# Kernel tuning notes

Hardware: AMD Instinct MI355X
Metric: run time of the kernel (lower is better)

## Reference

```python
import jax, jax.numpy as jnp
import numpy as np

EPS_BN = 1e-5
EPS_NORM = 1e-12
TEMPERATURE = 0.1
TEMPLATE_LAMBDA = 0.5
KERNEL_WIDTH = 5


def conv1d(x, w, b, pad):
    # x: (B, Cin, W), w: (Cout, Cin, K)
    y = jax.lax.conv_general_dilated(x, w, window_strides=(1,), padding=[(pad, pad)],
                                     dimension_numbers=('NCW', 'OIW', 'NCW'))
    return y + b[None, :, None]


def batchnorm(x, g, be):
    # training-mode BN: batch stats over (B, W), biased variance (as torch)
    m = jnp.mean(x, axis=(0, 2), keepdims=True)
    v = jnp.mean((x - m) ** 2, axis=(0, 2), keepdims=True)
    return g[None, :, None] * (x - m) * jax.lax.rsqrt(v + EPS_BN) + be[None, :, None]


def maxpool4(x):
    return jax.lax.reduce_window(x, -jnp.inf, jax.lax.max, (1, 1, 4), (1, 1, 4), 'VALID')


def adaptive_avg_pool1d(x, k):
    # faithful torch AdaptiveAvgPool1d bin boundaries
    W = x.shape[-1]
    outs = []
    for i in range(k):
        s = (i * W) // k
        e = -(-((i + 1) * W) // k)  # ceil
        outs.append(jnp.mean(x[..., s:e], axis=-1))
    return jnp.stack(outs, axis=-1)


def l2norm(x):
    n = jnp.linalg.norm(x, axis=-1, keepdims=True)
    return x / jnp.maximum(n, EPS_NORM)


def encoder(x, w1, b1, g1, be1, w2, b2, g2, be2, w3, b3, g3, be3):
    h = maxpool4(jax.nn.relu(batchnorm(conv1d(x, w1, b1, 8), g1, be1)))
    h = maxpool4(jax.nn.relu(batchnorm(conv1d(h, w2, b2, 8), g2, be2)))
    h = maxpool4(jax.nn.relu(batchnorm(conv1d(h, w3, b3, 8), g3, be3)))
    return h  # (B, C, W=L/64)


def template_head(h, tw1, tb1, tg1, tbe1, tw2, tb2, tg2, tbe2):
    k = jax.nn.relu(batchnorm(conv1d(h, tw1, tb1, 2), tg1, tbe1))
    k = jax.nn.relu(batchnorm(conv1d(k, tw2, tb2, 1), tg2, tbe2))
    return adaptive_avg_pool1d(k, KERNEL_WIDTH)  # (B, C, W_k)


def template_similarity(k, h):
    # Equivalent to the torch B*B*C grouped 'same' conv1d followed by
    # sum over channels and mean over positions: since the result is the
    # SUM over all output positions of a zero-padded cross-correlation,
    # it factorizes as einsum of k with shifted window-sums of h.
    k = k - jnp.mean(k, axis=-1, keepdims=True)
    k = l2norm(k)  # (B, C, Wk)
    h = h - jnp.mean(h, axis=-1, keepdims=True)
    h = l2norm(h)  # (B, C, W)
    Wk = k.shape[-1]
    W = h.shape[-1]
    pad = (Wk - 1) // 2  # padding='same' for odd kernel
    hp = jnp.pad(h, ((0, 0), (0, 0), (pad, pad)))
    # S[j,c,t] = sum_w hp[j,c,w+t]  for t in [0, Wk)
    S = jnp.stack([jnp.sum(hp[:, :, t:t + W], axis=-1) for t in range(Wk)], axis=-1)
    return jnp.einsum('ick,jck->ij', k, S) / W  # (B, B)


def infonce(sim):
    logp = jax.nn.log_softmax(sim / TEMPERATURE, axis=-1)
    return -jnp.mean(jnp.diagonal(logp))


def template_contrastive_loss(k1, k2):
    B = k1.shape[0]
    a = l2norm(k1.reshape(B, -1))
    b = l2norm(k2.reshape(B, -1))
    return infonce(jnp.matmul(a, b.T) * TEMPERATURE / TEMPERATURE) if False else infonce(jnp.matmul(a, b.T))


def setup_inputs() -> dict:
    key = jax.random.key(0)
    ks = jax.random.split(key, 12)
    B, L, C = 256, 8192, 64
    inp = {
        'x1': jax.random.normal(ks[0], (B, 1, L), dtype=jnp.float32),
        'x2': jax.random.normal(ks[1], (B, 1, L), dtype=jnp.float32),
        # encoder params
        'w1': jax.random.normal(ks[2], (16, 1, 17), dtype=jnp.float32) * 0.1,
        'b1': jnp.zeros((16,), jnp.float32),
        'g1': jnp.ones((16,), jnp.float32), 'be1': jnp.zeros((16,), jnp.float32),
        'w2': jax.random.normal(ks[3], (32, 16, 17), dtype=jnp.float32) * 0.05,
        'b2': jnp.zeros((32,), jnp.float32),
        'g2': jnp.ones((32,), jnp.float32), 'be2': jnp.zeros((32,), jnp.float32),
        'w3': jax.random.normal(ks[4], (C, 32, 17), dtype=jnp.float32) * 0.04,
        'b3': jnp.zeros((C,), jnp.float32),
        'g3': jnp.ones((C,), jnp.float32), 'be3': jnp.zeros((C,), jnp.float32),
        # template head params
        'tw1': jax.random.normal(ks[5], (C, C, 5), dtype=jnp.float32) * 0.05,
        'tb1': jnp.zeros((C,), jnp.float32),
        'tg1': jnp.ones((C,), jnp.float32), 'tbe1': jnp.zeros((C,), jnp.float32),
        'tw2': jax.random.normal(ks[6], (C, C, 3), dtype=jnp.float32) * 0.07,
        'tb2': jnp.zeros((C,), jnp.float32),
        'tg2': jnp.ones((C,), jnp.float32), 'tbe2': jnp.zeros((C,), jnp.float32),
    }
    return inp


def reference(x1, x2, w1, b1, g1, be1, w2, b2, g2, be2, w3, b3, g3, be3,
              tw1, tb1, tg1, tbe1, tw2, tb2, tg2, tbe2):
    enc = (w1, b1, g1, be1, w2, b2, g2, be2, w3, b3, g3, be3)
    th = (tw1, tb1, tg1, tbe1, tw2, tb2, tg2, tbe2)
    h1 = encoder(x1, *enc)
    h2 = encoder(x2, *enc)
    k1 = template_head(h1, *th)
    k2 = template_head(h2, *th)
    loss_matching = (infonce(template_similarity(k1, h2)) +
                     infonce(template_similarity(k2, h1))) / 2
    loss_template = template_contrastive_loss(k1, k2)
    return loss_matching + TEMPLATE_LAMBDA * loss_template
```

## Files before the change

### kernel.cpp

```cpp
#include <hip/hip_runtime.h>
#include <hip/hip_bf16.h>
#include <math.h>


#define BSZ2 512
#define NTHR 256

typedef __attribute__((ext_vector_type(8))) short bf16x8;
typedef __attribute__((ext_vector_type(4))) float f32x4;

static inline int ceil_divll(long long a, int b) { return (int)((a + b - 1) / b); }

__device__ __forceinline__ unsigned short f2bf(float f) {
    unsigned u = __float_as_uint(f);
    u = (u + 0x7FFFu + ((u >> 16) & 1u)) >> 16;
    return (unsigned short)u;
}
__device__ __forceinline__ float bflo(unsigned u) { return __uint_as_float(u << 16); }
__device__ __forceinline__ float bfhi(unsigned u) { return __uint_as_float(u & 0xFFFF0000u); }

template<int WT>
__global__ __launch_bounds__(256)
void conv1_mfma(const float* __restrict__ x1, const float* __restrict__ x2,
                const unsigned short* __restrict__ wpack1, const float* __restrict__ bias,
                unsigned short* __restrict__ outMax, unsigned short* __restrict__ outMin,
                float* __restrict__ partials)
{
    constexpr int W = 8192;
    constexpr int CHUNK = 4 * WT * 16;
    __shared__ float xs[CHUNK + 32];
    __shared__ float sred[4][16];
    __shared__ float ssred[4][16];

    const int tid = threadIdx.x;
    const int ntile = W / CHUNK;
    const int b = blockIdx.x / ntile;
    const int w0 = (blockIdx.x % ntile) * CHUNK;
    const float* xrow = (b < 256) ? x1 + (long long)b * W : x2 + (long long)(b - 256) * W;

    for (int i = tid; i < CHUNK + 32; i += 256) {
        const int gw = w0 - 8 + i;
        xs[i] = (gw >= 0 && gw < W) ? xrow[gw] : 0.f;
    }
    __syncthreads();

    const int lane = tid & 63, wave = tid >> 6;
    const int n = lane & 15, kq = lane >> 4;
    const bf16x8 a = *(const bf16x8*)(wpack1 + lane * 8);

    f32x4 acc[WT];
#pragma unroll
    for (int wt = 0; wt < WT; ++wt) { acc[wt][0]=0.f; acc[wt][1]=0.f; acc[wt][2]=0.f; acc[wt][3]=0.f; }

    const int base0 = wave * WT * 16 + n + kq * 8;
#pragma unroll
    for (int wt = 0; wt < WT; ++wt) {
        bf16x8 bv;
#pragma unroll
        for (int j = 0; j < 8; ++j) {
            __hip_bfloat16 h = __float2bfloat16(xs[base0 + wt * 16 + j]);
            bv[j] = *reinterpret_cast<const short*>(&h);
        }
        acc[wt] = __builtin_amdgcn_mfma_f32_16x16x32_bf16(bv, a, acc[wt], 0, 0, 0);
    }

    const float bi = bias[n];
    float s_ = 0.f, ss_ = 0.f;
#pragma unroll
    for (int wt = 0; wt < WT; ++wt) {
        float v[4];
#pragma unroll
        for (int e = 0; e < 4; ++e) {
            v[e] = acc[wt][e] + bi;
            s_ += v[e]; ss_ += v[e] * v[e];
        }
        const float mx = fmaxf(fmaxf(v[0], v[1]), fmaxf(v[2], v[3]));
        const float mn = fminf(fminf(v[0], v[1]), fminf(v[2], v[3]));
        const int wp = (w0 >> 2) + wave * WT * 4 + wt * 4 + kq;
        outMax[((long long)b * 2048 + wp) * 16 + n] = f2bf(mx);
        outMin[((long long)b * 2048 + wp) * 16 + n] = f2bf(mn);
    }
    s_  += __shfl_xor(s_, 16, 64);  s_  += __shfl_xor(s_, 32, 64);
    ss_ += __shfl_xor(ss_, 16, 64); ss_ += __shfl_xor(ss_, 32, 64);
    if (lane < 16) { sred[wave][n] = s_; ssred[wave][n] = ss_; }
    __syncthreads();
    if (tid < 16) {
        float sumv = 0.f, sumsq = 0.f;
#pragma unroll
        for (int wv = 0; wv < 4; ++wv) { sumv += sred[wv][tid]; sumsq += ssred[wv][tid]; }
        partials[((long long)blockIdx.x * 16 + tid) * 2 + 0] = sumv;
        partials[((long long)blockIdx.x * 16 + tid) * 2 + 1] = sumsq;
    }
}

template<int COUT>
__global__ void finalize2(const float* __restrict__ partials, int nblk_half, float invN,
                          const float* __restrict__ g, const float* __restrict__ be,
                          float* __restrict__ scale, float* __restrict__ shift)
{
    const int co = blockIdx.x;
    const int half = blockIdx.y;
    const float* P = partials + (size_t)half * nblk_half * COUT * 2;
    float s = 0.f, ss = 0.f;
    for (int i = threadIdx.x; i < nblk_half; i += NTHR) {
        s  += P[((long long)i * COUT + co) * 2 + 0];
        ss += P[((long long)i * COUT + co) * 2 + 1];
    }
    __shared__ float red[NTHR][2];
    red[threadIdx.x][0] = s; red[threadIdx.x][1] = ss;
    __syncthreads();
    for (int off = NTHR / 2; off > 0; off >>= 1) {
        if ((int)threadIdx.x < off) {
            red[threadIdx.x][0] += red[threadIdx.x + off][0];
            red[threadIdx.x][1] += red[threadIdx.x + off][1];
        }
        __syncthreads();
    }
    if (threadIdx.x == 0) {
        const float m = red[0][0] * invN;
        const float v = red[0][1] * invN - m * m;
        const float inv = rsqrtf(v + 1e-5f);
        const float sc = g[co] * inv;
        scale[half * COUT + co] = sc;
        shift[half * COUT + co] = be[co] - sc * m;
    }
}

template<int CIN, int KK, int DT, int NP, int S, int CT>
__device__ __forceinline__ void pack_one(int idx, const float* __restrict__ wgt,
                                         unsigned short* __restrict__ wp)
{
    const int j = idx & 7;
    const int l = (idx >> 3) & 63;
    int rest = idx >> 9;
    const int ct = rest % CT; rest /= CT;
    const int s = rest % S;
    const int p = rest / S;
    const int co = ct * 16 + (l & 15);
    const int k = (l >> 4) * 8 + j;
    int ci, t;
    if (DT == 2) { ci = k & (CIN - 1); t = p * 2 + (k >> 4); }
    else         { ci = s * 32 + k;    t = p; }
    float v = (t < KK) ? wgt[((long long)co * CIN + ci) * KK + t] : 0.f;
    wp[idx] = f2bf(v);
}

__global__ void build_all_wpacks(const float* __restrict__ w1, const float* __restrict__ w2,
                                 const float* __restrict__ w3,
                                 const float* __restrict__ tw1, const float* __restrict__ tw2,
                                 unsigned short* __restrict__ wp1,
                                 unsigned short* __restrict__ wp2, unsigned short* __restrict__ wp3,
                                 unsigned short* __restrict__ wpt1, unsigned short* __restrict__ wpt2)
{
    const int idx = blockIdx.x * NTHR + threadIdx.x;
    const int n1 = 512;
    const int n2 = 9 * 1 * 2 * 512;
    const int n3 = 17 * 1 * 4 * 512;
    const int nt1 = 5 * 2 * 4 * 512;
    const int nt2 = 3 * 2 * 4 * 512;
    if (idx < n1) {
        const int j = idx & 7, l = idx >> 3;
        const int co = l & 15, k = (l >> 4) * 8 + j;
        wp1[idx] = f2bf((k < 17) ? w1[co * 17 + k] : 0.f);
    }
    else if (idx < n1 + n2) pack_one<16, 17, 2, 9, 1, 2>(idx - n1, w2, wp2);
    else if (idx < n1 + n2 + n3) pack_one<32, 17, 1, 17, 1, 4>(idx - n1 - n2, w3, wp3);
    else if (idx < n1 + n2 + n3 + nt1) pack_one<64, 5, 1, 5, 2, 4>(idx - n1 - n2 - n3, tw1, wpt1);
    else if (idx < n1 + n2 + n3 + nt1 + nt2) pack_one<64, 3, 1, 3, 2, 4>(idx - n1 - n2 - n3 - nt1, tw2, wpt2);
}

template<int CIN, int COUT, int KK, int PAD, int DT, int NP, int S, int CT, int ST,
         int SRCM, int OUTM>
__global__ __launch_bounds__(256)
void conv_mfma2(const unsigned short* __restrict__ xA, const unsigned short* __restrict__ xB,
                const float* __restrict__ pscale, const float* __restrict__ pshift,
                const unsigned short* __restrict__ wpack, const float* __restrict__ bias,
                unsigned short* __restrict__ outA, unsigned short* __restrict__ outB,
                float* __restrict__ partials, int W)
{
    constexpr int CHUNK = 4 * ST * 16;
    constexpr int ROWB = CIN * 2 + 16;
    constexpr int ROWS = CHUNK + KK + (DT - 1) + 1;
    constexpr int DPR = CIN / 2;
    __shared__ __align__(16) unsigned char lx[ROWS * ROWB];
    __shared__ float sred[4][CT][16];
    __shared__ float ssred[4][CT][16];
    __shared__ float scb[(SRCM > 0) ? CIN : 1];
    __shared__ float shb[(SRCM > 0) ? CIN : 1];

    const int tid = threadIdx.x;
    const int ntile = W / CHUNK;
    const int b = blockIdx.x / ntile;
    const int tile = blockIdx.x % ntile;
    const int w0 = tile * CHUNK;

    if (SRCM > 0) {
        if (tid < CIN) {
            scb[tid] = pscale[(b >> 8) * CIN + tid];
            shb[tid] = pshift[(b >> 8) * CIN + tid];
        }
        __syncthreads();
    }

    for (int d = tid; d < ROWS * DPR; d += 256) {
        const int row = d / DPR;
        const int col = d % DPR;
        const int gw = w0 - PAD + row;
        unsigned v = 0;
        if (gw >= 0 && gw < W) {
            const long long src = ((long long)b * W + gw) * CIN + col * 2;
            if (SRCM == 0) {
                v = *(const unsigned*)(xA + src);
            } else {
                const unsigned va = *(const unsigned*)(xA + src);
                const float sc0 = scb[col * 2], sh0 = shb[col * 2];
                const float sc1 = scb[col * 2 + 1], sh1 = shb[col * 2 + 1];
                float f0, f1;
                if (SRCM == 1) {
                    const unsigned vb = *(const unsigned*)(xB + src);
                    f0 = fmaxf(fmaf(sc0, (sc0 > 0.f) ? bflo(va) : bflo(vb), sh0), 0.f);
                    f1 = fmaxf(fmaf(sc1, (sc1 > 0.f) ? bfhi(va) : bfhi(vb), sh1), 0.f);
                } else {
                    f0 = fmaxf(fmaf(sc0, bflo(va), sh0), 0.f);
                    f1 = fmaxf(fmaf(sc1, bfhi(va), sh1), 0.f);
                }
                v = (unsigned)f2bf(f0) | ((unsigned)f2bf(f1) << 16);
            }
        }
        *(unsigned*)(lx + row * ROWB + col * 4) = v;
    }
    __syncthreads();

    const int lane = tid & 63, wave = tid >> 6;
    const int n = lane & 15, kq = lane >> 4;
    int rowbase, cbyte;
    if (DT == 2) { rowbase = wave * ST * 16 + n + (kq >> 1); cbyte = (kq & 1) * 16; }
    else         { rowbase = wave * ST * 16 + n;             cbyte = kq * 16; }

    f32x4 acc[ST][CT];
#pragma unroll
    for (int st = 0; st < ST; ++st)
#pragma unroll
        for (int ct = 0; ct < CT; ++ct) { acc[st][ct][0]=0.f; acc[st][ct][1]=0.f; acc[st][ct][2]=0.f; acc[st][ct][3]=0.f; }

#pragma unroll
    for (int p = 0; p < NP; ++p) {
#pragma unroll
        for (int s = 0; s < S; ++s) {
            bf16x8 a[CT];
#pragma unroll
            for (int ct = 0; ct < CT; ++ct)
                a[ct] = *(const bf16x8*)(wpack + (((long long)(p * S + s) * CT + ct) * 64 + lane) * 8);
#pragma unroll
            for (int st = 0; st < ST; ++st) {
                const int r = rowbase + st * 16 + p * DT;
                const bf16x8 bf = *(const bf16x8*)(lx + r * ROWB + cbyte + s * 64);
#pragma unroll
                for (int ct = 0; ct < CT; ++ct)
                    acc[st][ct] = __builtin_amdgcn_mfma_f32_16x16x32_bf16(bf, a[ct], acc[st][ct], 0, 0, 0);
            }
        }
    }

    float s_[CT], ss_[CT];
#pragma unroll
    for (int ct = 0; ct < CT; ++ct) { s_[ct] = 0.f; ss_[ct] = 0.f; }

#pragma unroll
    for (int st = 0; st < ST; ++st) {
        const int wbase = w0 + wave * ST * 16 + st * 16 + kq * 4;
#pragma unroll
        for (int ct = 0; ct < CT; ++ct) {
            const float bi = bias[ct * 16 + n];
            float v[4];
#pragma unroll
            for (int e = 0; e < 4; ++e) {
                v[e] = acc[st][ct][e] + bi;
                s_[ct] += v[e];
                ss_[ct] += v[e] * v[e];
            }
            if (OUTM == 0) {
#pragma unroll
                for (int e = 0; e < 4; ++e)
                    outA[((long long)b * W + wbase + e) * COUT + ct * 16 + n] = f2bf(v[e]);
            } else {
                const float mx = fmaxf(fmaxf(v[0], v[1]), fmaxf(v[2], v[3]));
                const float mn = fminf(fminf(v[0], v[1]), fminf(v[2], v[3]));
                const long long o = ((long long)b * (W >> 2) + (wbase >> 2)) * COUT + ct * 16 + n;
                outA[o] = f2bf(mx);
                outB[o] = f2bf(mn);
            }
        }
    }
#pragma unroll
    for (int ct = 0; ct < CT; ++ct) {
        s_[ct]  += __shfl_xor(s_[ct], 16, 64);  s_[ct]  += __shfl_xor(s_[ct], 32, 64);
        ss_[ct] += __shfl_xor(ss_[ct], 16, 64); ss_[ct] += __shfl_xor(ss_[ct], 32, 64);
    }
    if (lane < 16) {
#pragma unroll
        for (int ct = 0; ct < CT; ++ct) { sred[wave][ct][n] = s_[ct]; ssred[wave][ct][n] = ss_[ct]; }
    }
    __syncthreads();
    if (tid < COUT) {
        const int ct = tid >> 4, nn = tid & 15;
        float sumv = 0.f, sumsq = 0.f;
#pragma unroll
        for (int wv = 0; wv < 4; ++wv) { sumv += sred[wv][ct][nn]; sumsq += ssred[wv][ct][nn]; }
        partials[((long long)blockIdx.x * COUT + tid) * 2 + 0] = sumv;
        partials[((long long)blockIdx.x * COUT + tid) * 2 + 1] = sumsq;
    }
}

__global__ void tail_pool_srow(const unsigned short* __restrict__ yT2b,
                               const float* __restrict__ scT2, const float* __restrict__ shT2,
                               const unsigned short* __restrict__ yMax3,
                               const unsigned short* __restrict__ yMin3,
                               const float* __restrict__ scS3, const float* __restrict__ shS3,
                               float* __restrict__ kn, float* __restrict__ ab,
                               float* __restrict__ Sv)
{
    __shared__ float hb[128][64];
    const int tid = threadIdx.x;
    if (blockIdx.x < BSZ2) {
        const int b = blockIdx.x;
        __shared__ float pk[320];
        __shared__ float red2[NTHR];
        const uint2* yd = (const uint2*)(yT2b + (long long)b * 128 * 64);
        for (int i = tid; i < 128 * 16; i += 256) {
            const int w = i >> 4, c4 = (i & 15) * 4;
            const float* scp = scT2 + (b >> 8) * 64 + c4;
            const float* shp = shT2 + (b >> 8) * 64 + c4;
            const uint2 v = yd[i];
            hb[w][c4 + 0] = fmaxf(fmaf(scp[0], bflo(v.x), shp[0]), 0.f);
            hb[w][c4 + 1] = fmaxf(fmaf(scp[1], bfhi(v.x), shp[1]), 0.f);
            hb[w][c4 + 2] = fmaxf(fmaf(scp[2], bflo(v.y), shp[2]), 0.f);
            hb[w][c4 + 3] = fmaxf(fmaf(scp[3], bfhi(v.y), shp[3]), 0.f);
        }
        __syncthreads();
        const int bs[5] = {0, 25, 51, 76, 102};
        const int be5[5] = {26, 52, 77, 103, 128};
        for (int o = tid; o < 320; o += 256) {
            const int cc = o & 63, bin = o >> 6;
            float acc = 0.f;
            for (int w = bs[bin]; w < be5[bin]; ++w) acc += hb[w][cc];
            pk[cc * 5 + bin] = acc / (float)(be5[bin] - bs[bin]);
        }
        __syncthreads();
        float n2p = pk[tid] * pk[tid];
        if (tid < 64) n2p += pk[256 + tid] * pk[256 + tid];
        red2[tid] = n2p;
        __syncthreads();
        for (int off = NTHR / 2; off > 0; off >>= 1) {
            if (tid < off) red2[tid] += red2[tid + off];
            __syncthreads();
        }
        const float nrm = fmaxf(sqrtf(red2[0]), 1e-12f);
        for (int i = tid; i < 320; i += 256) ab[(long long)b * 320 + i] = pk[i] / nrm;
        if (tid < 64) {
            const float* p = pk + tid * 5;
            float m = 0.f;
            for (int t = 0; t < 5; ++t) m += p[t];
            m *= 0.2f;
            float v[5]; float q = 0.f;
            for (int t = 0; t < 5; ++t) { v[t] = p[t] - m; q += v[t] * v[t]; }
            const float n = fmaxf(sqrtf(q), 1e-12f);
            float* o = kn + ((long long)b * 64 + tid) * 5;
            for (int t = 0; t < 5; ++t) o[t] = v[t] / n;
        }
    } else {
        __shared__ float red[4][64];
        __shared__ float mrow[64];
        const int b = blockIdx.x - BSZ2;
        const int c = tid & 63, grp = tid >> 6;
        const uint2* ya = (const uint2*)(yMax3 + (long long)b * 128 * 64);
        const uint2* yb = (const uint2*)(yMin3 + (long long)b * 128 * 64);
        for (int i = tid; i < 128 * 16; i += 256) {
            const int w = i >> 4, c4 = (i & 15) * 4;
            const float* scp = scS3 + (b >> 8) * 64 + c4;
            const float* shp = shS3 + (b >> 8) * 64 + c4;
            const uint2 va = ya[i], vb = yb[i];
            hb[w][c4 + 0] = fmaxf(fmaf(scp[0], (scp[0] > 0.f) ? bflo(va.x) : bflo(vb.x), shp[0]), 0.f);
            hb[w][c4 + 1] = fmaxf(fmaf(scp[1], (scp[1] > 0.f) ? bfhi(va.x) : bfhi(vb.x), shp[1]), 0.f);
            hb[w][c4 + 2] = fmaxf(fmaf(scp[2], (scp[2] > 0.f) ? bflo(va.y) : bflo(vb.y), shp[2]), 0.f);
            hb[w][c4 + 3] = fmaxf(fmaf(scp[3], (scp[3] > 0.f) ? bfhi(va.y) : bfhi(vb.y), shp[3]), 0.f);
        }
        __syncthreads();
        float s = 0.f;
        for (int w = grp * 32; w < grp * 32 + 32; ++w) s += hb[w][c];
        red[grp][c] = s;
        __syncthreads();
        if (tid < 64) mrow[tid] = (red[0][tid] + red[1][tid] + red[2][tid] + red[3][tid]) / 128.f;
        __syncthreads();
        const float m = mrow[c];
        float q = 0.f;
        for (int w = grp * 32; w < grp * 32 + 32; ++w) { const float d = hb[w][c] - m; q += d * d; }
        red[grp][c] = q;
        __syncthreads();
        if (tid < 64) {
            const float n2 = red[0][tid] + red[1][tid] + red[2][tid] + red[3][tid];
            const float n = fmaxf(sqrtf(n2), 1e-12f);
            const float m0 = mrow[tid];
            const float h0 = (hb[0][tid] - m0) / n, h1 = (hb[1][tid] - m0) / n;
            const float hN1 = (hb[127][tid] - m0) / n, hN2 = (hb[126][tid] - m0) / n;
            float* o = Sv + ((long long)b * 64 + tid) * 5;
            o[0] = -(hN2 + hN1); o[1] = -hN1; o[2] = 0.f; o[3] = -h0; o[4] = -(h0 + h1);
        }
    }
}

__global__ void simdot_nce(const float* __restrict__ kn, const float* __restrict__ Sv,
                           const float* __restrict__ ab, float* __restrict__ lp)
{
    const int j = threadIdx.x;
    const int i = blockIdx.x;
    const int z = blockIdx.y;
    const float* a;
    const float* b;
    float coef;
    if (z == 0)      { a = kn + (long long)i * 320;         b = Sv + (long long)(256 + j) * 320; coef = 10.f / 128.f; }
    else if (z == 1) { a = kn + (long long)(256 + i) * 320; b = Sv + (long long)j * 320;         coef = 10.f / 128.f; }
    else             { a = ab + (long long)i * 320;         b = ab + (long long)(256 + j) * 320; coef = 10.f; }
    const float4* a4 = (const float4*)a;
    const float4* b4 = (const float4*)b;
    float acc = 0.f;
#pragma unroll 8
    for (int d = 0; d < 80; ++d) {
        const float4 xv = a4[d], yv = b4[d];
        acc += xv.x * yv.x + xv.y * yv.y + xv.z * yv.z + xv.w * yv.w;
    }
    const float v = acc * coef;

    __shared__ float red[NTHR];
    __shared__ float sdiag;
    if (j == i) sdiag = v;
    red[j] = v;
    __syncthreads();
    for (int off = NTHR / 2; off > 0; off >>= 1) {
        if (j < off) red[j] = fmaxf(red[j], red[j + off]);
        __syncthreads();
    }
    const float mx = red[0];
    __syncthreads();
    red[j] = expf(v - mx);
    __syncthreads();
    for (int off = NTHR / 2; off > 0; off >>= 1) {
        if (j < off) red[j] += red[j + off];
        __syncthreads();
    }
    if (j == 0) lp[z * 256 + i] = sdiag - (mx + logf(red[0]));
}

__global__ void final3(const float* __restrict__ lp, float* __restrict__ out)
{
    __shared__ float red[NTHR];
    const int tid = threadIdx.x;
    float l[3];
    for (int z = 0; z < 3; ++z) {
        red[tid] = lp[z * 256 + tid];
        __syncthreads();
        for (int off = NTHR / 2; off > 0; off >>= 1) {
            if (tid < off) red[tid] += red[tid + off];
            __syncthreads();
        }
        l[z] = red[0];
        __syncthreads();
    }
    if (tid == 0)
        out[0] = 0.5f * (-l[0] / 256.f - l[1] / 256.f) + 0.5f * (-l[2] / 256.f);
}


extern "C" void kernel_launch(void* const* d_in, const int* in_sizes, int n_in,
                              void* d_out, int out_size, void* d_ws, size_t ws_size,
                              hipStream_t stream)
{
    const float* x1  = (const float*)d_in[0];
    const float* x2  = (const float*)d_in[1];
    const float* w1  = (const float*)d_in[2];
    const float* b1  = (const float*)d_in[3];
    const float* g1  = (const float*)d_in[4];
    const float* be1 = (const float*)d_in[5];
    const float* w2  = (const float*)d_in[6];
    const float* b2  = (const float*)d_in[7];
    const float* g2  = (const float*)d_in[8];
    const float* be2 = (const float*)d_in[9];
    const float* w3  = (const float*)d_in[10];
    const float* b3  = (const float*)d_in[11];
    const float* g3  = (const float*)d_in[12];
    const float* be3 = (const float*)d_in[13];
    const float* tw1 = (const float*)d_in[14];
    const float* tb1 = (const float*)d_in[15];
    const float* tg1 = (const float*)d_in[16];
    const float* tbe1= (const float*)d_in[17];
    const float* tw2 = (const float*)d_in[18];
    const float* tb2 = (const float*)d_in[19];
    const float* tg2 = (const float*)d_in[20];
    const float* tbe2= (const float*)d_in[21];
    float* out = (float*)d_out;

    char* ws = (char*)d_ws;
    size_t off = 0;
    auto alloc = [&](size_t bytes) -> void* {
        off = (off + 255) & ~(size_t)255;
        void* p = ws + off;
        off += bytes;
        return p;
    };
    typedef unsigned short u16;
    u16* yMax1 = (u16*)alloc((size_t)BSZ2 * 2048 * 16 * 2);
    u16* yMin1 = (u16*)alloc((size_t)BSZ2 * 2048 * 16 * 2);
    u16* yMax2 = (u16*)alloc((size_t)BSZ2 * 512 * 32 * 2);
    u16* yMin2 = (u16*)alloc((size_t)BSZ2 * 512 * 32 * 2);
    u16* yMax3 = (u16*)alloc((size_t)BSZ2 * 128 * 64 * 2);
    u16* yMin3 = (u16*)alloc((size_t)BSZ2 * 128 * 64 * 2);
    u16* yT1   = (u16*)alloc((size_t)BSZ2 * 128 * 64 * 2);
    u16* yT2b  = (u16*)alloc((size_t)BSZ2 * 128 * 64 * 2);
    u16* wp1  = (u16*)alloc((size_t)512 * 2);
    u16* wp2  = (u16*)alloc((size_t)9 * 1 * 2 * 512 * 2);
    u16* wp3  = (u16*)alloc((size_t)17 * 1 * 4 * 512 * 2);
    u16* wpt1 = (u16*)alloc((size_t)5 * 2 * 4 * 512 * 2);
    u16* wpt2 = (u16*)alloc((size_t)3 * 2 * 4 * 512 * 2);
    float* kn   = (float*)alloc((size_t)BSZ2 * 320 * 4);
    float* ab   = (float*)alloc((size_t)BSZ2 * 320 * 4);
    float* Sv   = (float*)alloc((size_t)BSZ2 * 320 * 4);
    float* lp   = (float*)alloc((size_t)3 * 256 * 4);
    float* partials = (float*)alloc((size_t)16384 * 16 * 2 * 4);
    float* scales = (float*)alloc((size_t)5 * 128 * 4);
    float* shifts = (float*)alloc((size_t)5 * 128 * 4);
    float* sc1 = scales + 0 * 128, * sh1 = shifts + 0 * 128;
    float* sc2 = scales + 1 * 128, * sh2 = shifts + 1 * 128;
    float* sc3 = scales + 2 * 128, * sh3 = shifts + 2 * 128;
    float* sct1 = scales + 3 * 128, * sht1 = shifts + 3 * 128;
    float* sct2 = scales + 4 * 128, * sht2 = shifts + 4 * 128;

    build_all_wpacks<<<303, NTHR, 0, stream>>>(w1, w2, w3, tw1, tw2, wp1, wp2, wp3, wpt1, wpt2);

    {
        const int nblk = BSZ2 * (8192 / 512);
        conv1_mfma<8><<<nblk, 256, 0, stream>>>(x1, x2, wp1, b1, yMax1, yMin1, partials);
        dim3 fg(16, 2);
        finalize2<16><<<fg, NTHR, 0, stream>>>(partials, nblk / 2, 1.f / (256.f * 8192.f), g1, be1, sc1, sh1);
    }
    {
        const int nblk = BSZ2 * (2048 / 256);
        conv_mfma2<16,32,17,8,2,9,1,2,4, 1,1><<<nblk, 256, 0, stream>>>(
            yMax1, yMin1, sc1, sh1, wp2, b2, yMax2, yMin2, partials, 2048);
        dim3 fg(32, 2);
        finalize2<32><<<fg, NTHR, 0, stream>>>(partials, nblk / 2, 1.f / (256.f * 2048.f), g2, be2, sc2, sh2);
    }
    {
        const int nblk = BSZ2 * (512 / 256);
        conv_mfma2<32,64,17,8,1,17,1,4,4, 1,1><<<nblk, 256, 0, stream>>>(
            yMax2, yMin2, sc2, sh2, wp3, b3, yMax3, yMin3, partials, 512);
        dim3 fg(64, 2);
        finalize2<64><<<fg, NTHR, 0, stream>>>(partials, nblk / 2, 1.f / (256.f * 512.f), g3, be3, sc3, sh3);
    }
    {
        conv_mfma2<64,64,5,2,1,5,2,4,2, 1,0><<<BSZ2, 256, 0, stream>>>(
            yMax3, yMin3, sc3, sh3, wpt1, tb1, yT1, nullptr, partials, 128);
        dim3 fg(64, 2);
        finalize2<64><<<fg, NTHR, 0, stream>>>(partials, 256, 1.f / (256.f * 128.f), tg1, tbe1, sct1, sht1);
    }
    {
        conv_mfma2<64,64,3,1,1,3,2,4,2, 2,0><<<BSZ2, 256, 0, stream>>>(
            yT1, nullptr, sct1, sht1, wpt2, tb2, yT2b, nullptr, partials, 128);
        dim3 fg(64, 2);
        finalize2<64><<<fg, NTHR, 0, stream>>>(partials, 256, 1.f / (256.f * 128.f), tg2, tbe2, sct2, sht2);
    }

    tail_pool_srow<<<2 * BSZ2, 256, 0, stream>>>(yT2b, sct2, sht2, yMax3, yMin3, sc3, sh3, kn, ab, Sv);
    dim3 sg(256, 3);
    simdot_nce<<<sg, NTHR, 0, stream>>>(kn, Sv, ab, lp);
    final3<<<1, NTHR, 0, stream>>>(lp, out);
}
```

Before: 187.9 us.

## Fuse conv1 recompute into conv2 kernel, dropping conv1 intermediate buffers

```diff
diff --git a/kernel.cpp b/kernel.cpp
--- a/kernel.cpp
+++ b/kernel.cpp
@@ -21,10 +21,9 @@
 
 template<int WT>
 __global__ __launch_bounds__(256)
-void conv1_mfma(const float* __restrict__ x1, const float* __restrict__ x2,
-                const unsigned short* __restrict__ wpack1, const float* __restrict__ bias,
-                unsigned short* __restrict__ outMax, unsigned short* __restrict__ outMin,
-                float* __restrict__ partials)
+void conv1_stats(const float* __restrict__ x1, const float* __restrict__ x2,
+                 const unsigned short* __restrict__ wpack1, const float* __restrict__ bias,
+                 float* __restrict__ partials)
 {
     constexpr int W = 8192;
     constexpr int CHUNK = 4 * WT * 16;
@@ -48,10 +47,8 @@
     const int n = lane & 15, kq = lane >> 4;
     const bf16x8 a = *(const bf16x8*)(wpack1 + lane * 8);
 
-    f32x4 acc[WT];
-#pragma unroll
-    for (int wt = 0; wt < WT; ++wt) { acc[wt][0]=0.f; acc[wt][1]=0.f; acc[wt][2]=0.f; acc[wt][3]=0.f; }
-
+    const float bi = bias[n];
+    float s_ = 0.f, ss_ = 0.f;
     const int base0 = wave * WT * 16 + n + kq * 8;
 #pragma unroll
     for (int wt = 0; wt < WT; ++wt) {
@@ -61,24 +58,13 @@
             __hip_bfloat16 h = __float2bfloat16(xs[base0 + wt * 16 + j]);
             bv[j] = *reinterpret_cast<const short*>(&h);
         }
-        acc[wt] = __builtin_amdgcn_mfma_f32_16x16x32_bf16(bv, a, acc[wt], 0, 0, 0);
-    }
-
-    const float bi = bias[n];
-    float s_ = 0.f, ss_ = 0.f;
-#pragma unroll
-    for (int wt = 0; wt < WT; ++wt) {
-        float v[4];
+        f32x4 acc = {0.f, 0.f, 0.f, 0.f};
+        acc = __builtin_amdgcn_mfma_f32_16x16x32_bf16(bv, a, acc, 0, 0, 0);
 #pragma unroll
         for (int e = 0; e < 4; ++e) {
-            v[e] = acc[wt][e] + bi;
-            s_ += v[e]; ss_ += v[e] * v[e];
-        }
-        const float mx = fmaxf(fmaxf(v[0], v[1]), fmaxf(v[2], v[3]));
-        const float mn = fminf(fminf(v[0], v[1]), fminf(v[2], v[3]));
-        const int wp = (w0 >> 2) + wave * WT * 4 + wt * 4 + kq;
-        outMax[((long long)b * 2048 + wp) * 16 + n] = f2bf(mx);
-        outMin[((long long)b * 2048 + wp) * 16 + n] = f2bf(mn);
+            const float y = acc[e] + bi;
+            s_ += y; ss_ += y * y;
+        }
     }
     s_  += __shfl_xor(s_, 16, 64);  s_  += __shfl_xor(s_, 32, 64);
     ss_ += __shfl_xor(ss_, 16, 64); ss_ += __shfl_xor(ss_, 32, 64);
@@ -90,6 +76,144 @@
         for (int wv = 0; wv < 4; ++wv) { sumv += sred[wv][tid]; sumsq += ssred[wv][tid]; }
         partials[((long long)blockIdx.x * 16 + tid) * 2 + 0] = sumv;
         partials[((long long)blockIdx.x * 16 + tid) * 2 + 1] = sumsq;
+    }
+}
+
+__global__ __launch_bounds__(256)
+void conv12_fused(const float* __restrict__ x1, const float* __restrict__ x2,
+                  const unsigned short* __restrict__ wpack1, const float* __restrict__ b1v,
+                  const float* __restrict__ sc1, const float* __restrict__ sh1,
+                  const unsigned short* __restrict__ wp2, const float* __restrict__ b2v,
+                  unsigned short* __restrict__ outMax, unsigned short* __restrict__ outMin,
+                  float* __restrict__ partials)
+{
+    constexpr int W2 = 2048;
+    constexpr int CHUNK = 256;
+    constexpr int ST = 4, CT = 2, NP = 9, KK = 17;
+    constexpr int CIN = 16, COUT = 32;
+    constexpr int ROWB = CIN * 2 + 16;
+    constexpr int ROWS = CHUNK + KK + 1 + 1;
+    constexpr int XLEN = 1136;
+    __shared__ float xs[XLEN];
+    __shared__ __align__(16) unsigned char lx[ROWS * ROWB];
+    __shared__ float sred[4][CT][16];
+    __shared__ float ssred[4][CT][16];
+
+    const int tid = threadIdx.x;
+    const int b = blockIdx.x >> 3;
+    const int tile = blockIdx.x & 7;
+    const int w0 = tile * CHUNK;
+    const int half = b >> 8;
+    const float* xrow = (b < 256) ? x1 + (long long)b * 8192 : x2 + (long long)(b - 256) * 8192;
+    const int xbase = 4 * w0 - 40;
+
+    for (int i = tid; i < XLEN; i += 256) {
+        const int gx = xbase + i;
+        xs[i] = (gx >= 0 && gx < 8192) ? xrow[gx] : 0.f;
+    }
+    __syncthreads();
+
+    const int lane = tid & 63, wave = tid >> 6;
+    const int n = lane & 15, kq = lane >> 4;
+
+    {
+        const bf16x8 a1 = *(const bf16x8*)(wpack1 + lane * 8);
+        const float bi1 = b1v[n];
+        const float scv = sc1[half * 16 + n];
+        const float shv = sh1[half * 16 + n];
+        for (int i = 0; i < 18; ++i) {
+            const int g = wave + 4 * i;
+            if (g >= 69) break;
+            bf16x8 bv;
+#pragma unroll
+            for (int j = 0; j < 8; ++j) {
+                __hip_bfloat16 h = __float2bfloat16(xs[16 * g + n + kq * 8 + j]);
+                bv[j] = *reinterpret_cast<const short*>(&h);
+            }
+            f32x4 acc = {0.f, 0.f, 0.f, 0.f};
+            acc = __builtin_amdgcn_mfma_f32_16x16x32_bf16(bv, a1, acc, 0, 0, 0);
+            const float t0 = fmaf(scv, acc[0] + bi1, shv);
+            const float t1 = fmaf(scv, acc[1] + bi1, shv);
+            const float t2 = fmaf(scv, acc[2] + bi1, shv);
+            const float t3 = fmaf(scv, acc[3] + bi1, shv);
+            const float pooled = fmaxf(fmaxf(fmaxf(t0, t1), fmaxf(t2, t3)), 0.f);
+            const int row_local = 4 * g + kq;
+            const int r_global = (w0 - 8) + row_local;
+            if (row_local < ROWS) {
+                const unsigned short val =
+                    (r_global >= 0 && r_global < W2) ? f2bf(pooled) : (unsigned short)0;
+                *(unsigned short*)(lx + row_local * ROWB + n * 2) = val;
+            }
+        }
+    }
+    __syncthreads();
+
+    const int rowbase = wave * ST * 16 + n + (kq >> 1);
+    const int cbyte = (kq & 1) * 16;
+
+    f32x4 acc2[ST][CT];
+#pragma unroll
+    for (int st = 0; st < ST; ++st)
+#pragma unroll
+        for (int ct = 0; ct < CT; ++ct) { acc2[st][ct][0]=0.f; acc2[st][ct][1]=0.f; acc2[st][ct][2]=0.f; acc2[st][ct][3]=0.f; }
+
+#pragma unroll
+    for (int p = 0; p < NP; ++p) {
+        bf16x8 a[CT];
+#pragma unroll
+        for (int ct = 0; ct < CT; ++ct)
+            a[ct] = *(const bf16x8*)(wp2 + (((long long)p * CT + ct) * 64 + lane) * 8);
+#pragma unroll
+        for (int st = 0; st < ST; ++st) {
+            const int r = rowbase + st * 16 + p * 2;
+            const bf16x8 bf = *(const bf16x8*)(lx + r * ROWB + cbyte);
+#pragma unroll
+            for (int ct = 0; ct < CT; ++ct)
+                acc2[st][ct] = __builtin_amdgcn_mfma_f32_16x16x32_bf16(bf, a[ct], acc2[st][ct], 0, 0, 0);
+        }
+    }
+
+    float s_[CT], ss_[CT];
+#pragma unroll
+    for (int ct = 0; ct < CT; ++ct) { s_[ct] = 0.f; ss_[ct] = 0.f; }
+
+#pragma unroll
+    for (int st = 0; st < ST; ++st) {
+        const int wbase = w0 + wave * ST * 16 + st * 16 + kq * 4;
+#pragma unroll
+        for (int ct = 0; ct < CT; ++ct) {
+            const float bi = b2v[ct * 16 + n];
+            float v[4];
+#pragma unroll
+            for (int e = 0; e < 4; ++e) {
+                v[e] = acc2[st][ct][e] + bi;
+                s_[ct] += v[e];
+                ss_[ct] += v[e] * v[e];
+            }
+            const float mx = fmaxf(fmaxf(v[0], v[1]), fmaxf(v[2], v[3]));
+            const float mn = fminf(fminf(v[0], v[1]), fminf(v[2], v[3]));
+            const long long o = ((long long)b * (W2 >> 2) + (wbase >> 2)) * COUT + ct * 16 + n;
+            outMax[o] = f2bf(mx);
+            outMin[o] = f2bf(mn);
+        }
+    }
+#pragma unroll
+    for (int ct = 0; ct < CT; ++ct) {
+        s_[ct]  += __shfl_xor(s_[ct], 16, 64);  s_[ct]  += __shfl_xor(s_[ct], 32, 64);
+        ss_[ct] += __shfl_xor(ss_[ct], 16, 64); ss_[ct] += __shfl_xor(ss_[ct], 32, 64);
+    }
+    if (lane < 16) {
+#pragma unroll
+        for (int ct = 0; ct < CT; ++ct) { sred[wave][ct][n] = s_[ct]; ssred[wave][ct][n] = ss_[ct]; }
+    }
+    __syncthreads();
+    if (tid < COUT) {
+        const int ct = tid >> 4, nn = tid & 15;
+        float sumv = 0.f, sumsq = 0.f;
+#pragma unroll
+        for (int wv = 0; wv < 4; ++wv) { sumv += sred[wv][ct][nn]; sumsq += ssred[wv][ct][nn]; }
+        partials[((long long)blockIdx.x * COUT + tid) * 2 + 0] = sumv;
+        partials[((long long)blockIdx.x * COUT + tid) * 2 + 1] = sumsq;
     }
 }
 
@@ -508,8 +632,6 @@
         return p;
     };
     typedef unsigned short u16;
-    u16* yMax1 = (u16*)alloc((size_t)BSZ2 * 2048 * 16 * 2);
-    u16* yMin1 = (u16*)alloc((size_t)BSZ2 * 2048 * 16 * 2);
     u16* yMax2 = (u16*)alloc((size_t)BSZ2 * 512 * 32 * 2);
     u16* yMin2 = (u16*)alloc((size_t)BSZ2 * 512 * 32 * 2);
     u16* yMax3 = (u16*)alloc((size_t)BSZ2 * 128 * 64 * 2);
@@ -538,14 +660,14 @@
 
     {
         const int nblk = BSZ2 * (8192 / 512);
-        conv1_mfma<8><<<nblk, 256, 0, stream>>>(x1, x2, wp1, b1, yMax1, yMin1, partials);
+        conv1_stats<8><<<nblk, 256, 0, stream>>>(x1, x2, wp1, b1, partials);
         dim3 fg(16, 2);
         finalize2<16><<<fg, NTHR, 0, stream>>>(partials, nblk / 2, 1.f / (256.f * 8192.f), g1, be1, sc1, sh1);
     }
     {
-        const int nblk = BSZ2 * (2048 / 256);
-        conv_mfma2<16,32,17,8,2,9,1,2,4, 1,1><<<nblk, 256, 0, stream>>>(
-            yMax1, yMin1, sc1, sh1, wp2, b2, yMax2, yMin2, partials, 2048);
+        const int nblk = BSZ2 * 8;
+        conv12_fused<<<nblk, 256, 0, stream>>>(x1, x2, wp1, b1, sc1, sh1,
+                                               wp2, b2, yMax2, yMin2, partials);
         dim3 fg(32, 2);
         finalize2<32><<<fg, NTHR, 0, stream>>>(partials, nblk / 2, 1.f / (256.f * 2048.f), g2, be2, sc2, sh2);
     }
```

New measurement: 184.7 us, median of 2. Within noise of the previous version (-1.7%).
